# Kernel optimization log

Measured on AMD Instinct MI355X. Metric: run time of the kernel, lower is better.

## Reference

```python
import jax, jax.numpy as jnp
import numpy as np

KS = 3  # 3x3 windows at dilations 1 and 3; center of d=3 window dropped -> 17 taps


def conv1x1(x, w, b=None):
    # x: (N, C, H, W), w: (O, C)
    y = jnp.einsum('nchw,oc->nohw', x, w)
    if b is not None:
        y = y + b[None, :, None, None]
    return y


def unfold3(x, d):
    # F.unfold(kernel=3, stride=1, dilation=d, padding=d) -> (N, C, 9, H, W)
    N, C, H, W = x.shape
    xp = jnp.pad(x, ((0, 0), (0, 0), (d, d), (d, d)))
    cols = [xp[:, :, i * d:i * d + H, j * d:j * d + W]
            for i in range(KS) for j in range(KS)]
    return jnp.stack(cols, axis=2)


def neighborhoods(feat):
    # 9 taps at dilation 1 + 8 taps at dilation 3 (center removed) -> (N, C, 17, H, W)
    u1 = unfold3(feat, 1)
    u3 = unfold3(feat, 3)
    u3 = jnp.concatenate([u3[:, :, :4], u3[:, :, 5:]], axis=2)
    return jnp.concatenate([u1, u3], axis=2)


def setup_inputs() -> dict:
    key = jax.random.key(0)
    ks = jax.random.split(key, 16)
    F_, C, H, W = 8, 128, 96, 96
    I = 64
    s = 0.05
    d = {
        'x': jax.random.normal(ks[0], (F_, C, H, W), jnp.float32),
        'rgb': jax.random.normal(ks[1], (1, C, H, W), jnp.float32),
        'g_w': jax.random.normal(ks[2], (I, C), jnp.float32) * s,
        'g_b': jax.random.normal(ks[3], (I,), jnp.float32) * s,
        'theta_w': jax.random.normal(ks[4], (I, C), jnp.float32) * s,
        'theta_b': jax.random.normal(ks[5], (I,), jnp.float32) * s,
        'phi_w': jax.random.normal(ks[6], (I, C), jnp.float32) * s,
        'phi_b': jax.random.normal(ks[7], (I,), jnp.float32) * s,
        'W_w': jax.random.normal(ks[8], (C, I), jnp.float32) * s,
        'W_b': jax.random.normal(ks[9], (C,), jnp.float32) * s,
        'rgb_g_w': jax.random.normal(ks[10], (I, C), jnp.float32) * s,
        'rgb_g_b': jnp.zeros((I,), jnp.float32),
        'rgb_theta_w': jax.random.normal(ks[11], (I, C), jnp.float32) * s,
        'rgb_theta_b': jnp.zeros((I,), jnp.float32),
        'rgb_phi_w': jax.random.normal(ks[12], (I, C), jnp.float32) * s,
        'rgb_phi_b': jnp.zeros((I,), jnp.float32),
        'rgb_W_w': jax.random.normal(ks[13], (C, I), jnp.float32) * s,
        'rgb_W_b': jax.random.normal(ks[14], (C,), jnp.float32) * s,
        'cp_w': jax.random.normal(ks[15], (2 * I,), jnp.float32) * s,
    }
    return d


def reference(x, rgb, g_w, g_b, theta_w, theta_b, phi_w, phi_b, W_w, W_b,
              rgb_g_w, rgb_g_b, rgb_theta_w, rgb_theta_b, rgb_phi_w, rgb_phi_b,
              rgb_W_w, rgb_W_b, cp_w):
    F_, C, H, W = x.shape
    P = H * W
    I = g_w.shape[0]
    T = 17  # neighborhood taps

    # ----- x (focal-stack) branch: softmax attention over F_*17 keys per pixel -----
    g = neighborhoods(conv1x1(x, g_w, g_b)).reshape(F_, I, T, P)
    g = g.transpose(3, 0, 2, 1).reshape(P, F_ * T, I)            # (P, F*17, I)
    th = neighborhoods(conv1x1(x, theta_w, theta_b)).reshape(F_, I, T, P)
    th = th.transpose(3, 1, 0, 2).reshape(P, I, F_ * T)          # (P, I, F*17)
    ph = conv1x1(x, phi_w, phi_b).reshape(F_, I, P).transpose(2, 0, 1)  # (P, F, I)

    f = jnp.einsum('pfc,pck->pfk', ph, th)                       # (P, F, F*17)
    attn = jax.nn.softmax(f, axis=-1)
    y = jnp.einsum('pfk,pkc->pfc', attn, g)                      # (P, F, I)
    y = y.transpose(1, 2, 0).reshape(F_, I, H, W)
    W_y = conv1x1(y, W_w, W_b)

    # ----- rgb branch: concat-projection scores (relu of additive logits) / 17 -----
    g_r = neighborhoods(conv1x1(rgb, rgb_g_w, rgb_g_b)).reshape(1, I, T, P)[0]
    g_r = g_r.transpose(2, 1, 0)                                 # (P, 17, I)
    th_r = neighborhoods(conv1x1(rgb, rgb_theta_w, rgb_theta_b)).reshape(1, I, T, P)[0]  # (I,17,P)
    ph_r = conv1x1(x, rgb_phi_w, rgb_phi_b).reshape(F_, I, P)    # (F, I, P)

    # concat_project is a 1x1 conv (2I->1, no bias) + ReLU over cat([theta_rep, phi_rep]);
    # equivalent to relu(wt.theta + wp.phi) without materializing the repeated concat.
    wt, wp = cp_w[:I], cp_w[I:]
    a = jnp.einsum('c,ctp->pt', wt, th_r)                        # (P, 17)
    b = jnp.einsum('c,fcp->pf', wp, ph_r)                        # (P, F)
    f_r = jax.nn.relu(a[:, None, :] + b[:, :, None]) / T         # (P, F, 17)
    y_r = jnp.einsum('pft,pti->pfi', f_r, g_r)                   # (P, F, I)
    y_r = y_r.transpose(1, 2, 0).reshape(F_, I, H, W)
    W_y_r = conv1x1(y_r, rgb_W_w, rgb_W_b)

    return W_y + W_y_r + x
```

## Files before the change

### kernel.cpp

```cpp
#include <hip/hip_runtime.h>

#define F_ 8
#define C_ 128
#define C2_ (C_/2)
#define H_ 96
#define W_ 96
#define P_ (H_*W_)
#define I_ 64
#define I2_ (I_/2)
#define T_ 17
#define KK_ (F_*T_)

__device__ constexpr int DY[T_] = {-1,-1,-1, 0,0,0, 1,1,1, -3,-3,-3, 0,0, 3,3,3};
__device__ constexpr int DX[T_] = {-1, 0, 1,-1,0,1,-1,0,1, -3, 0, 3,-3,3,-3,0,3};

__constant__ int CDY[T_] = {-3,-3,-3, -1,-1,-1,  0, 0,0,0, 0,  1,1,1,  3, 3, 3};
__constant__ int CDX[T_] = {-3, 0, 3, -1, 0, 1, -3,-1,0,1, 3, -1,0,1, -3, 0, 3};
__constant__ int CK [T_] = { 9,10,11,  0, 1, 2, 12, 3,4,5,13,  6,7,8, 14,15,16};

typedef unsigned short u16;
typedef u16 u16x8 __attribute__((ext_vector_type(8)));
typedef short s16x8 __attribute__((ext_vector_type(8)));
typedef float f32x2 __attribute__((ext_vector_type(2)));
typedef float f32x4 __attribute__((ext_vector_type(4)));
typedef _Float16 h16x2 __attribute__((ext_vector_type(2)));
typedef _Float16 h16x8 __attribute__((ext_vector_type(8)));

__device__ __forceinline__ float b2f(u16 u) { return __uint_as_float(((unsigned)u) << 16); }
__device__ __forceinline__ u16 f2b(float f) {
    unsigned u = __float_as_uint(f);
    u += 0x7fff + ((u >> 16) & 1);
    return (u16)(u >> 16);
}
__device__ __forceinline__ h16x2 u2h(unsigned u) {
    union { unsigned u; h16x2 h; } x; x.u = u; return x.h;
}
__device__ __forceinline__ unsigned packh(float a, float b) {
    union { unsigned u; h16x2 h; } x;
    x.h[0] = (_Float16)a; x.h[1] = (_Float16)b; return x.u;
}
__device__ __forceinline__ float dot2(h16x2 a, h16x2 b, float c) {
#if __has_builtin(__builtin_amdgcn_fdot2)
    return __builtin_amdgcn_fdot2(a, b, c, false);
#else
    return c + (float)a[0] * (float)b[0] + (float)a[1] * (float)b[1];
#endif
}

__global__ __launch_bounds__(128) void k_prep(const float* __restrict__ rtw,
                                              const float* __restrict__ rpw,
                                              const float* __restrict__ rtb,
                                              const float* __restrict__ rpb,
                                              const float* __restrict__ cp,
                                              float* __restrict__ vt,
                                              float* __restrict__ u,
                                              float* __restrict__ ct,
                                              unsigned* __restrict__ uh) {
    __shared__ float su[C_];
    int c = threadIdx.x;
    float a = 0.f, b2 = 0.f;
    for (int i = 0; i < I_; ++i) {
        a  += cp[i]      * rtw[i*C_ + c];
        b2 += cp[I_ + i] * rpw[i*C_ + c];
    }
    vt[c] = a; u[c] = b2; su[c] = b2;
    if (c == 0) { float s = 0.f; for (int i = 0; i < I_; ++i) s += cp[i]      * rtb[i]; ct[0] = s; }
    if (c == 1) { float s = 0.f; for (int i = 0; i < I_; ++i) s += cp[I_ + i] * rpb[i]; ct[1] = s; }
    __syncthreads();
    if (c < C2_) uh[c] = packh(su[2*c], su[2*c+1]);
}

__global__ __launch_bounds__(256) void k_tr(const float* __restrict__ rg_w,
                                            float* __restrict__ rgT) {
    int idx = blockIdx.x * 256 + threadIdx.x;
    int r = idx / C_, c = idx % C_;
    rgT[c*I_ + r] = rg_w[idx];
}

__global__ __launch_bounds__(256) void k_wpk(const float* __restrict__ g_w,
                                             const float* __restrict__ th_w,
                                             const float* __restrict__ ph_w,
                                             const float* __restrict__ g_b,
                                             const float* __restrict__ th_b,
                                             const float* __restrict__ ph_b,
                                             const float* __restrict__ u,
                                             const float* __restrict__ ct,
                                             _Float16* __restrict__ Wpk,
                                             float* __restrict__ ball) {
    int idx = blockIdx.x * 256 + threadIdx.x;
    if (idx < 26624) {
        int j    = idx & 7;
        int frag = idx >> 3;
        int l    = frag & 63;
        int t    = frag >> 6;
        int ks   = t & 3;
        int nt   = t >> 2;
        int c = ks * 32 + ((l >> 4) << 3) + j;
        int n = nt * 16 + (l & 15);
        float v;
        if (n < 192) {
            int proj = n >> 6, i = n & 63;
            const float* src = proj == 0 ? g_w : (proj == 1 ? th_w : ph_w);
            v = src[i * C_ + c];
        } else if (n == 192) v = u[c];
        else v = 0.f;
        Wpk[idx] = (_Float16)v;
    }
    if (idx < 208) {
        float b;
        if (idx < 192) {
            int proj = idx >> 6, i = idx & 63;
            const float* bs = proj == 0 ? g_b : (proj == 1 ? th_b : ph_b);
            b = bs[i];
        } else if (idx == 192) b = ct[1];
        else b = 0.f;
        ball[idx] = b;
    }
}

__global__ __launch_bounds__(256) void k_wpk2(const float* __restrict__ W_w,
                                              const float* __restrict__ rW_w,
                                              const float* __restrict__ Wb,
                                              const float* __restrict__ rWb,
                                              u16* __restrict__ Wpk2,
                                              float* __restrict__ ball2) {
    int idx = blockIdx.x * 256 + threadIdx.x;
    if (idx < 16384) {
        int j    = idx & 7;
        int frag = idx >> 3;
        int l    = frag & 63;
        int t    = frag >> 6;
        int ks   = t & 3;
        int nt   = t >> 2;
        int k = ks * 32 + ((l >> 4) << 3) + j;
        int n = nt * 16 + (l & 15);
        float v = (k < 64) ? W_w[n * I_ + k] : rW_w[n * I_ + (k - 64)];
        Wpk2[idx] = f2b(v);
    }
    if (idx < C_) ball2[idx] = Wb[idx] + rWb[idx];
}

__global__ __launch_bounds__(256) void k_xhT(const float* __restrict__ x,
                                             _Float16* __restrict__ xhT) {
    int p  = blockIdx.x * 256 + threadIdx.x;
    int cb = blockIdx.y;
    int f  = blockIdx.z;
    const float* xp = x + ((size_t)f * C_ + cb * 32) * P_ + p;
    unsigned r[16];
#pragma unroll
    for (int jj = 0; jj < 16; ++jj) {
        float a = xp[(size_t)(2 * jj)     * P_];
        float b = xp[(size_t)(2 * jj + 1) * P_];
        r[jj] = packh(a, b);
    }
    unsigned* dst = (unsigned*)(xhT + ((size_t)f * P_ + p) * C_ + cb * 32);
#pragma unroll
    for (int q4 = 0; q4 < 4; ++q4) {
        uint4 v; v.x = r[q4*4]; v.y = r[q4*4+1]; v.z = r[q4*4+2]; v.w = r[q4*4+3];
        *(uint4*)(dst + q4 * 4) = v;
    }
}

__global__ __launch_bounds__(256) void k_projm(const _Float16* __restrict__ xhT,
                                               const h16x8* __restrict__ Wpk,
                                               const float* __restrict__ ball,
                                               unsigned* __restrict__ oG,
                                               unsigned* __restrict__ oT,
                                               unsigned* __restrict__ oP,
                                               float* __restrict__ Bf) {
    int wid  = threadIdx.x >> 6;
    int lane = threadIdx.x & 63;
    int px0  = blockIdx.x * 64 + wid * 16;
    int f    = blockIdx.z;
    int lm   = lane & 15;
    int lg   = lane >> 4;
    const _Float16* xrow = xhT + ((size_t)f * P_ + px0 + lm) * C_ + lg * 8;
    h16x8 bfrag[4];
#pragma unroll
    for (int ks = 0; ks < 4; ++ks)
        bfrag[ks] = *(const h16x8*)(xrow + ks * 32);
#pragma unroll 1
    for (int nt = 0; nt < 13; ++nt) {
        f32x4 acc = {0.f, 0.f, 0.f, 0.f};
#pragma unroll
        for (int ks = 0; ks < 4; ++ks) {
            h16x8 afrag = Wpk[(nt * 4 + ks) * 64 + lane];
            acc = __builtin_amdgcn_mfma_f32_16x16x32_f16(afrag, bfrag[ks], acc, 0, 0, 0);
        }
        int nb = nt * 16 + lg * 4;
        if (nb < 192) {
            int proj = nb >> 6, i = nb & 63, i2 = i >> 1;
            unsigned* o = proj == 0 ? oG : (proj == 1 ? oT : oP);
            size_t base = ((size_t)f * I2_ + i2) * P_ + px0 + lm;
            o[base]      = packh(acc[0] + ball[nb],     acc[1] + ball[nb + 1]);
            o[base + P_] = packh(acc[2] + ball[nb + 2], acc[3] + ball[nb + 3]);
        } else if (nb == 192) {
            Bf[(size_t)f * P_ + px0 + lm] = acc[0] + ball[192];
        }
    }
}

__global__ __launch_bounds__(256) void k_rg(const float* __restrict__ rgb,
                                            const float* __restrict__ rgT,
                                            const float* __restrict__ rg_b,
                                            const float* __restrict__ vt,
                                            const float* __restrict__ ct,
                                            float* __restrict__ GR,
                                            float* __restrict__ SR) {
    int p = blockIdx.x * 256 + threadIdx.x;
    int y = blockIdx.y;
    if (y == 4) {
        float s = ct[0];
        for (int c = 0; c < C_; ++c) s += rgb[(size_t)c * P_ + p] * vt[c];
        SR[p] = s;
        return;
    }
    int i0 = y * 16;
    float acc[16];
#pragma unroll
    for (int ii = 0; ii < 16; ++ii) acc[ii] = 0.f;
#pragma unroll 2
    for (int c = 0; c < C_; ++c) {
        float xv = rgb[(size_t)c * P_ + p];
        const float* wr = rgT + (size_t)c * I_ + i0;
#pragma unroll
        for (int ii = 0; ii < 16; ++ii) acc[ii] += xv * wr[ii];
    }
#pragma unroll
    for (int ii = 0; ii < 16; ++ii) GR[(size_t)(i0 + ii) * P_ + p] = acc[ii] + rg_b[i0 + ii];
}

__global__ __launch_bounds__(256) void k_scores(const unsigned* __restrict__ PHu,
                                                const unsigned* __restrict__ THu,
                                                u16* __restrict__ S) {
    int p  = blockIdx.x * 256 + threadIdx.x;
    int k0 = blockIdx.y * 4;
    int px = p % W_, py = p / W_;
    size_t tb[4]; float msk[4];
#pragma unroll
    for (int kk = 0; kk < 4; ++kk) {
        int k  = k0 + kk;
        int f2 = k / T_;
        int t  = k - f2 * T_;
        int dy = DY[t], dx = DX[t];
        bool v = ((unsigned)(py + dy) < H_) && ((unsigned)(px + dx) < W_);
        int q  = p + dy * W_ + dx;
        q = min(max(q, 0), P_ - 1);
        tb[kk]  = (size_t)f2 * I2_ * P_ + q;
        msk[kk] = v ? 1.f : 0.f;
    }
    float acc[8][4];
#pragma unroll
    for (int a = 0; a < 8; ++a)
#pragma unroll
        for (int b = 0; b < 4; ++b) acc[a][b] = 0.f;
#pragma unroll 2
    for (int i2 = 0; i2 < I2_; ++i2) {
        h16x2 ph[8];
#pragma unroll
        for (int f1 = 0; f1 < 8; ++f1)
            ph[f1] = u2h(PHu[((size_t)f1 * I2_ + i2) * P_ + p]);
        h16x2 tv[4];
#pragma unroll
        for (int kk = 0; kk < 4; ++kk)
            tv[kk] = u2h(THu[tb[kk] + (size_t)i2 * P_]);
#pragma unroll
        for (int kk = 0; kk < 4; ++kk)
#pragma unroll
            for (int f1 = 0; f1 < 8; ++f1)
                acc[f1][kk] = dot2(ph[f1], tv[kk], acc[f1][kk]);
    }
#pragma unroll
    for (int kk = 0; kk < 4; ++kk) {
        u16x8 r;
#pragma unroll
        for (int f1 = 0; f1 < 8; ++f1) r[f1] = f2b(__expf(acc[f1][kk] * msk[kk]));
        *(u16x8*)(S + ((size_t)(k0 + kk) * P_ + p) * 8) = r;
    }
}

__global__ __launch_bounds__(256) void k_y(const u16* __restrict__ S,
                                           const u16* __restrict__ G,
                                           u16* __restrict__ Yp,
                                           float* __restrict__ DEN) {
    int p   = blockIdx.x * 256 + threadIdx.x;
    int ib  = blockIdx.y;
    int qtr = blockIdx.z;
    int px = p % W_, py = p / W_;
    const unsigned* Gu = (const unsigned*)G;
    f32x2 acc2[8][4];
    float den[8];
#pragma unroll
    for (int a = 0; a < 8; ++a) {
        den[a] = 0.f;
#pragma unroll
        for (int b = 0; b < 4; ++b) acc2[a][b] = 0.f;
    }
#pragma unroll 1
    for (int f2 = qtr * 2; f2 < qtr * 2 + 2; ++f2) {
        const unsigned* Gb = Gu + ((size_t)f2 * I2_ + ib * 4) * P_;
#pragma unroll 1
        for (int t = 0; t < T_; ++t) {
            int dy = CDY[t], dx = CDX[t], k = CK[t];
            bool v = ((unsigned)(py + dy) < H_) && ((unsigned)(px + dx) < W_);
            int q  = p + dy * W_ + dx;
            q = min(max(q, 0), P_ - 1);
            float mt = v ? 1.f : 0.f;
            f32x2 mt2; mt2[0] = mt; mt2[1] = mt;
            u16x8 svv = *(const u16x8*)(S + ((size_t)(f2 * T_ + k) * P_ + p) * 8);
            float sv[8];
#pragma unroll
            for (int ff = 0; ff < 8; ++ff) sv[ff] = b2f(svv[ff]);
            f32x2 gv2[4];
#pragma unroll
            for (int jj = 0; jj < 4; ++jj) {
                h16x2 h = u2h(Gb[(size_t)jj * P_ + q]);
                f32x2 g; g[0] = (float)h[0]; g[1] = (float)h[1];
                gv2[jj] = g * mt2;
            }
#pragma unroll
            for (int ff = 0; ff < 8; ++ff) {
                den[ff] += sv[ff];
                f32x2 s2; s2[0] = sv[ff]; s2[1] = sv[ff];
#pragma unroll
                for (int jj = 0; jj < 4; ++jj)
                    acc2[ff][jj] += s2 * gv2[jj];
            }
        }
    }
    if (blockIdx.y == 0) {
#pragma unroll
        for (int ff = 0; ff < 8; ++ff)
            DEN[(size_t)(qtr * F_ + ff) * P_ + p] = den[ff];
    }
    u16* Yh = Yp + (size_t)qtr * F_ * P_ * I_;
#pragma unroll
    for (int ff = 0; ff < 8; ++ff) {
        u16x8 r;
#pragma unroll
        for (int ii = 0; ii < 8; ++ii) r[ii] = f2b(acc2[ff][ii >> 1][ii & 1]);
        *(u16x8*)(Yh + (((size_t)ff * 8 + ib) * P_ + p) * 8) = r;
    }
}

__global__ __launch_bounds__(128) void k_yr(const float* __restrict__ SR,
                                            const float* __restrict__ Bf,
                                            const float* __restrict__ GR,
                                            u16* __restrict__ Yr) {
    int p  = blockIdx.x * 128 + threadIdx.x;
    int ib = blockIdx.y;
    int i0 = ib * 8;
    int px = p % W_, py = p / W_;
    float bfv[8];
#pragma unroll
    for (int f = 0; f < 8; ++f) bfv[f] = Bf[f * P_ + p];
    f32x2 acc2[8][4];
#pragma unroll
    for (int a = 0; a < 8; ++a)
#pragma unroll
        for (int b = 0; b < 4; ++b) acc2[a][b] = 0.f;
#pragma unroll
    for (int t = 0; t < T_; ++t) {
        int dy = DY[t], dx = DX[t];
        bool v = ((unsigned)(py + dy) < H_) && ((unsigned)(px + dx) < W_);
        int q  = p + dy * W_ + dx;
        q = min(max(q, 0), P_ - 1);
        float sr = SR[q];
        f32x2 gr2[4];
#pragma unroll
        for (int jj = 0; jj < 4; ++jj) {
            f32x2 g;
            g[0] = GR[(size_t)(i0 + 2*jj)     * P_ + q];
            g[1] = GR[(size_t)(i0 + 2*jj + 1) * P_ + q];
            gr2[jj] = g;
        }
#pragma unroll
        for (int f = 0; f < 8; ++f) {
            float fv = v ? fmaxf(sr + bfv[f], 0.f) * (1.f / (float)T_) : 0.f;
            f32x2 f2v; f2v[0] = fv; f2v[1] = fv;
#pragma unroll
            for (int jj = 0; jj < 4; ++jj) acc2[f][jj] += f2v * gr2[jj];
        }
    }
#pragma unroll
    for (int f = 0; f < 8; ++f) {
        u16x8 r;
#pragma unroll
        for (int ii = 0; ii < 8; ++ii) r[ii] = f2b(acc2[f][ii >> 1][ii & 1]);
        *(u16x8*)(Yr + (((size_t)f * 8 + ib) * P_ + p) * 8) = r;
    }
}

__global__ __launch_bounds__(256) void k_fold(const u16* __restrict__ Yp,
                                              const float* __restrict__ DEN,
                                              u16* __restrict__ Ys) {
    int p  = blockIdx.x * 256 + threadIdx.x;
    int i8 = blockIdx.y;
    int f  = blockIdx.z;
    float dv = 1.f / (DEN[(size_t)f * P_ + p]
                    + DEN[(size_t)(F_ + f) * P_ + p]
                    + DEN[(size_t)(2 * F_ + f) * P_ + p]
                    + DEN[(size_t)(3 * F_ + f) * P_ + p]);
    const size_t FPI = (size_t)F_ * P_ * I_;
    size_t base = (((size_t)f * 8 + i8) * P_ + p) * 8;
    u16x8 q0 = *(const u16x8*)(Yp + base);
    u16x8 q1 = *(const u16x8*)(Yp + FPI + base);
    u16x8 q2 = *(const u16x8*)(Yp + 2 * FPI + base);
    u16x8 q3 = *(const u16x8*)(Yp + 3 * FPI + base);
    u16x8 r;
#pragma unroll
    for (int j = 0; j < 8; ++j)
        r[j] = f2b((b2f(q0[j]) + b2f(q1[j]) + b2f(q2[j]) + b2f(q3[j])) * dv);
    *(u16x8*)(Ys + base) = r;
}

__global__ __launch_bounds__(256) void k_finalm(const u16* __restrict__ Ys,
                                                const u16* __restrict__ Yr,
                                                const s16x8* __restrict__ Wpk2,
                                                const float* __restrict__ ball2,
                                                const float* __restrict__ x,
                                                float* __restrict__ out) {
    int wid  = threadIdx.x >> 6;
    int lane = threadIdx.x & 63;
    int px0  = blockIdx.x * 64 + wid * 16;
    int f    = blockIdx.y;
    int lm   = lane & 15;
    int lg   = lane >> 4;
    s16x8 bfrag[4];
#pragma unroll
    for (int ks = 0; ks < 4; ++ks) {
        int ip = ks * 32 + lg * 8;
        const u16* src = (ip < 64) ? Ys : Yr;
        int ib = (ip & 63) >> 3;
        bfrag[ks] = *(const s16x8*)(src + (((size_t)f * 8 + ib) * P_ + px0 + lm) * 8);
    }
#pragma unroll 1
    for (int nt = 0; nt < 8; ++nt) {
        f32x4 acc = {0.f, 0.f, 0.f, 0.f};
#pragma unroll
        for (int ks = 0; ks < 4; ++ks) {
            s16x8 afrag = Wpk2[(nt * 4 + ks) * 64 + lane];
            acc = __builtin_amdgcn_mfma_f32_16x16x32_bf16(afrag, bfrag[ks], acc, 0, 0, 0);
        }
        int nb = nt * 16 + lg * 4;
#pragma unroll
        for (int r = 0; r < 4; ++r) {
            int c = nb + r;
            size_t o = ((size_t)f * C_ + c) * P_ + px0 + lm;
            out[o] = acc[r] + ball2[c] + x[o];
        }
    }
}

extern "C" void kernel_launch(void* const* d_in, const int* in_sizes, int n_in,
                              void* d_out, int out_size, void* d_ws, size_t ws_size,
                              hipStream_t stream) {
    const float* x    = (const float*)d_in[0];
    const float* rgb  = (const float*)d_in[1];
    const float* g_w  = (const float*)d_in[2];
    const float* g_b  = (const float*)d_in[3];
    const float* th_w = (const float*)d_in[4];
    const float* th_b = (const float*)d_in[5];
    const float* ph_w = (const float*)d_in[6];
    const float* ph_b = (const float*)d_in[7];
    const float* W_w  = (const float*)d_in[8];
    const float* W_b  = (const float*)d_in[9];
    const float* rg_w = (const float*)d_in[10];
    const float* rg_b = (const float*)d_in[11];
    const float* rt_w = (const float*)d_in[12];
    const float* rt_b = (const float*)d_in[13];
    const float* rp_w = (const float*)d_in[14];
    const float* rp_b = (const float*)d_in[15];
    const float* rW_w = (const float*)d_in[16];
    const float* rW_b = (const float*)d_in[17];
    const float* cp_w = (const float*)d_in[18];
    float* out = (float*)d_out;

    const size_t FIP = (size_t)F_ * I_ * P_;
    const size_t SKP = (size_t)F_ * KK_ * P_;

    u16* Gb  = (u16*)d_ws;
    u16* THb = Gb  + FIP;
    u16* PHb = THb + FIP;
    u16* Sb  = PHb + FIP;
    u16* Yp  = Sb  + SKP;
    u16* Yr  = Yp  + 4 * FIP;
    float* GR  = (float*)(Yr + FIP);
    float* SR  = GR + (size_t)I_ * P_;
    float* Bf  = SR + P_;
    float* DEN = Bf + (size_t)F_ * P_;
    float* VT  = DEN + 4 * (size_t)F_ * P_;
    float* U   = VT + C_;
    float* CT  = U + C_;
    unsigned* UH   = (unsigned*)(CT + 16);
    float* rgT = (float*)(UH + C2_);
    float* BALL = rgT + (size_t)C_ * I_;
    _Float16* WPK = (_Float16*)(BALL + 256);
    u16* WPK2   = (u16*)(WPK + 26624);
    float* BALL2 = (float*)(WPK2 + 16384);
    u16* Ysum = Gb;
    _Float16* XHT = (_Float16*)Yp;

    k_prep<<<1, 128, 0, stream>>>(rt_w, rp_w, rt_b, rp_b, cp_w, VT, U, CT, UH);
    k_tr<<<32, 256, 0, stream>>>(rg_w, rgT);
    k_wpk<<<104, 256, 0, stream>>>(g_w, th_w, ph_w, g_b, th_b, ph_b, U, CT, WPK, BALL);
    k_wpk2<<<64, 256, 0, stream>>>(W_w, rW_w, W_b, rW_b, WPK2, BALL2);

    k_xhT<<<dim3(P_ / 256, 4, F_), 256, 0, stream>>>(x, XHT);

    k_projm<<<dim3(P_ / 64, 1, F_), 256, 0, stream>>>(XHT, (const h16x8*)WPK, BALL,
                                                      (unsigned*)Gb, (unsigned*)THb,
                                                      (unsigned*)PHb, Bf);

    k_rg<<<dim3(P_ / 256, 5), 256, 0, stream>>>(rgb, rgT, rg_b, VT, CT, GR, SR);

    k_scores<<<dim3(P_ / 256, KK_ / 4), 256, 0, stream>>>((const unsigned*)PHb,
                                                          (const unsigned*)THb, Sb);

    k_y<<<dim3(P_ / 256, I_ / 8, 4), 256, 0, stream>>>(Sb, Gb, Yp, DEN);

    k_yr<<<dim3(P_ / 128, I_ / 8), 128, 0, stream>>>(SR, Bf, GR, Yr);

    k_fold<<<dim3(P_ / 256, 8, F_), 256, 0, stream>>>(Yp, DEN, Ysum);

    k_finalm<<<dim3(P_ / 64, F_), 256, 0, stream>>>(Ysum, Yr, (const s16x8*)WPK2,
                                                    BALL2, x, out);
}
```

Measured before the change: 178.6 us.

## Store projections in 8-channel interleaved blocks for vectorized 16-byte loads

Changes the layout of the g/theta/phi projection outputs from channel-pair planes to blocks of 8 channels contiguous per pixel. The projection kernel now writes 8-byte stores, and the score and aggregation kernels read 16-byte vectors instead of several strided 4-byte loads. This is meant to cut the number of memory transactions in the gather-heavy kernels. The cost is larger per-thread loads and more register pressure, and the projm stores become strided across lanes.

After: 168.2 us. 1.06x faster.

```diff
diff --git a/kernel.cpp b/kernel.cpp
--- a/kernel.cpp
+++ b/kernel.cpp
@@ -38,6 +38,9 @@
 __device__ __forceinline__ unsigned packh(float a, float b) {
     union { unsigned u; h16x2 h; } x;
     x.h[0] = (_Float16)a; x.h[1] = (_Float16)b; return x.u;
+}
+__device__ __forceinline__ h16x2 slice2(h16x8 v, int j) {
+    h16x2 r; r[0] = v[2*j]; r[1] = v[2*j+1]; return r;
 }
 __device__ __forceinline__ float dot2(h16x2 a, h16x2 b, float c) {
 #if __has_builtin(__builtin_amdgcn_fdot2)
@@ -164,9 +167,9 @@
 __global__ __launch_bounds__(256) void k_projm(const _Float16* __restrict__ xhT,
                                                const h16x8* __restrict__ Wpk,
                                                const float* __restrict__ ball,
-                                               unsigned* __restrict__ oG,
-                                               unsigned* __restrict__ oT,
-                                               unsigned* __restrict__ oP,
+                                               u16* __restrict__ oG,
+                                               u16* __restrict__ oT,
+                                               u16* __restrict__ oP,
                                                float* __restrict__ Bf) {
     int wid  = threadIdx.x >> 6;
     int lane = threadIdx.x & 63;
@@ -189,11 +192,14 @@
         }
         int nb = nt * 16 + lg * 4;
         if (nb < 192) {
-            int proj = nb >> 6, i = nb & 63, i2 = i >> 1;
-            unsigned* o = proj == 0 ? oG : (proj == 1 ? oT : oP);
-            size_t base = ((size_t)f * I2_ + i2) * P_ + px0 + lm;
-            o[base]      = packh(acc[0] + ball[nb],     acc[1] + ball[nb + 1]);
-            o[base + P_] = packh(acc[2] + ball[nb + 2], acc[3] + ball[nb + 3]);
+            int proj = nb >> 6, i = nb & 63;
+            int ib = i >> 3, i7 = i & 7;
+            u16* o = proj == 0 ? oG : (proj == 1 ? oT : oP);
+            size_t base = (((size_t)f * 8 + ib) * P_ + px0 + lm) * 8 + i7;
+            uint2 v;
+            v.x = packh(acc[0] + ball[nb],     acc[1] + ball[nb + 1]);
+            v.y = packh(acc[2] + ball[nb + 2], acc[3] + ball[nb + 3]);
+            *(uint2*)(o + base) = v;
         } else if (nb == 192) {
             Bf[(size_t)f * P_ + px0 + lm] = acc[0] + ball[192];
         }
@@ -230,13 +236,13 @@
     for (int ii = 0; ii < 16; ++ii) GR[(size_t)(i0 + ii) * P_ + p] = acc[ii] + rg_b[i0 + ii];
 }
 
-__global__ __launch_bounds__(256) void k_scores(const unsigned* __restrict__ PHu,
-                                                const unsigned* __restrict__ THu,
+__global__ __launch_bounds__(256) void k_scores(const u16* __restrict__ PH,
+                                                const u16* __restrict__ TH,
                                                 u16* __restrict__ S) {
     int p  = blockIdx.x * 256 + threadIdx.x;
     int k0 = blockIdx.y * 4;
     int px = p % W_, py = p / W_;
-    size_t tb[4]; float msk[4];
+    int qs[4], f2s[4]; float msk[4];
 #pragma unroll
     for (int kk = 0; kk < 4; ++kk) {
         int k  = k0 + kk;
@@ -246,7 +252,7 @@
         bool v = ((unsigned)(py + dy) < H_) && ((unsigned)(px + dx) < W_);
         int q  = p + dy * W_ + dx;
         q = min(max(q, 0), P_ - 1);
-        tb[kk]  = (size_t)f2 * I2_ * P_ + q;
+        qs[kk] = q; f2s[kk] = f2;
         msk[kk] = v ? 1.f : 0.f;
     }
     float acc[8][4];
@@ -254,21 +260,25 @@
     for (int a = 0; a < 8; ++a)
 #pragma unroll
         for (int b = 0; b < 4; ++b) acc[a][b] = 0.f;
-#pragma unroll 2
-    for (int i2 = 0; i2 < I2_; ++i2) {
-        h16x2 ph[8];
+#pragma unroll 1
+    for (int ib = 0; ib < 8; ++ib) {
+        h16x8 ph8[8];
 #pragma unroll
         for (int f1 = 0; f1 < 8; ++f1)
-            ph[f1] = u2h(PHu[((size_t)f1 * I2_ + i2) * P_ + p]);
-        h16x2 tv[4];
-#pragma unroll
-        for (int kk = 0; kk < 4; ++kk)
-            tv[kk] = u2h(THu[tb[kk] + (size_t)i2 * P_]);
-#pragma unroll
-        for (int kk = 0; kk < 4; ++kk)
-#pragma unroll
-            for (int f1 = 0; f1 < 8; ++f1)
-                acc[f1][kk] = dot2(ph[f1], tv[kk], acc[f1][kk]);
+            ph8[f1] = *(const h16x8*)(PH + (((size_t)f1 * 8 + ib) * P_ + p) * 8);
+#pragma unroll
+        for (int kk = 0; kk < 4; ++kk) {
+            h16x8 th8 = *(const h16x8*)(TH + (((size_t)f2s[kk] * 8 + ib) * P_ + qs[kk]) * 8);
+            h16x2 t0 = slice2(th8, 0), t1 = slice2(th8, 1),
+                  t2 = slice2(th8, 2), t3 = slice2(th8, 3);
+#pragma unroll
+            for (int f1 = 0; f1 < 8; ++f1) {
+                acc[f1][kk] = dot2(slice2(ph8[f1], 0), t0, acc[f1][kk]);
+                acc[f1][kk] = dot2(slice2(ph8[f1], 1), t1, acc[f1][kk]);
+                acc[f1][kk] = dot2(slice2(ph8[f1], 2), t2, acc[f1][kk]);
+                acc[f1][kk] = dot2(slice2(ph8[f1], 3), t3, acc[f1][kk]);
+            }
+        }
     }
 #pragma unroll
     for (int kk = 0; kk < 4; ++kk) {
@@ -287,7 +297,6 @@
     int ib  = blockIdx.y;
     int qtr = blockIdx.z;
     int px = p % W_, py = p / W_;
-    const unsigned* Gu = (const unsigned*)G;
     f32x2 acc2[8][4];
     float den[8];
 #pragma unroll
@@ -298,7 +307,7 @@
     }
 #pragma unroll 1
     for (int f2 = qtr * 2; f2 < qtr * 2 + 2; ++f2) {
-        const unsigned* Gb = Gu + ((size_t)f2 * I2_ + ib * 4) * P_;
+        const u16* Gb = G + (((size_t)f2 * 8 + ib) * P_) * 8;
 #pragma unroll 1
         for (int t = 0; t < T_; ++t) {
             int dy = CDY[t], dx = CDX[t], k = CK[t];
@@ -311,11 +320,11 @@
             float sv[8];
 #pragma unroll
             for (int ff = 0; ff < 8; ++ff) sv[ff] = b2f(svv[ff]);
+            h16x8 gh = *(const h16x8*)(Gb + (size_t)q * 8);
             f32x2 gv2[4];
 #pragma unroll
             for (int jj = 0; jj < 4; ++jj) {
-                h16x2 h = u2h(Gb[(size_t)jj * P_ + q]);
-                f32x2 g; g[0] = (float)h[0]; g[1] = (float)h[1];
+                f32x2 g; g[0] = (float)gh[2*jj]; g[1] = (float)gh[2*jj+1];
                 gv2[jj] = g * mt2;
             }
 #pragma unroll
@@ -509,13 +518,11 @@
     k_xhT<<<dim3(P_ / 256, 4, F_), 256, 0, stream>>>(x, XHT);
 
     k_projm<<<dim3(P_ / 64, 1, F_), 256, 0, stream>>>(XHT, (const h16x8*)WPK, BALL,
-                                                      (unsigned*)Gb, (unsigned*)THb,
-                                                      (unsigned*)PHb, Bf);
+                                                      Gb, THb, PHb, Bf);
 
     k_rg<<<dim3(P_ / 256, 5), 256, 0, stream>>>(rgb, rgT, rg_b, VT, CT, GR, SR);
 
-    k_scores<<<dim3(P_ / 256, KK_ / 4), 256, 0, stream>>>((const unsigned*)PHb,
-                                                          (const unsigned*)THb, Sb);
+    k_scores<<<dim3(P_ / 256, KK_ / 4), 256, 0, stream>>>(PHb, THb, Sb);
 
     k_y<<<dim3(P_ / 256, I_ / 8, 4), 256, 0, stream>>>(Sb, Gb, Yp, DEN);
 
```
